# Kernel optimization log

Measured on AMD Instinct MI355X. Metric: run time of the kernel, lower is better.

## Reference

```python
import jax, jax.numpy as jnp
import numpy as np

EPS = 1e-5
D, H, W = 2, 4, 4          # fixed patch grid from the rearrange string
P = 8                       # p1*p2*p3 = 2*2*2 tokens per patch


def setup_inputs() -> dict:
    key = jax.random.key(0)
    k1, k2, k3, k4, k5 = jax.random.split(key, 5)
    c, heads = 128, 8
    B = 16 * D * H * W  # 512 patches (b=16)
    emb = jax.random.normal(k1, (B, P, c), dtype=jnp.float32)
    s = 1.0 / np.sqrt(c)
    Wq = jax.random.normal(k2, (c, c * heads), dtype=jnp.float32) * s
    Wk = jax.random.normal(k3, (c, c * heads), dtype=jnp.float32) * s
    Wv = jax.random.normal(k4, (c, c * heads), dtype=jnp.float32) * s
    Wout = jax.random.normal(k5, (c * heads, c), dtype=jnp.float32) * (1.0 / np.sqrt(c * heads))
    return {"emb": emb, "Wq": Wq, "Wk": Wk, "Wv": Wv, "Wout": Wout}


def reference(emb, Wq, Wk, Wv, Wout):
    B, n, c = emb.shape            # B = b*32, n = 8
    heads = Wq.shape[1] // c
    b = B // (D * H * W)

    q = emb @ Wq                   # (B, 8, c*heads)
    k = emb @ Wk
    v = emb @ Wv

    # '(p) (c heads)' -> heads c p  /  heads p c
    mh_q = q.reshape(B, P, c, heads).transpose(0, 3, 2, 1)   # (B, heads, c, P)
    mh_k = k.reshape(B, P, c, heads).transpose(0, 3, 1, 2)   # (B, heads, P, c)
    mh_v = v.reshape(B, P, c, heads).transpose(0, 3, 2, 1)   # (B, heads, c, P)

    attn = jnp.einsum('bhcp,bhpe->bhce', mh_q, mh_k)         # (B, heads, c, c) channel scores

    # InstanceNorm2d(num_heads): normalize each (patch, head) c x c map (biased var)
    mu = attn.mean(axis=(2, 3), keepdims=True)
    var = attn.var(axis=(2, 3), keepdims=True)
    attn = (attn - mu) * jax.lax.rsqrt(var + EPS)

    attn = jax.nn.softmax(attn, axis=3)
    ctx = jnp.einsum('bhce,bhep->bhcp', attn, mh_v)          # (B, heads, c, P)

    # '(b d h w) heads c (p1 p2 p3) -> b (d p1 h p2 w p3) (c heads)'
    ctx = ctx.reshape(b, D, H, W, heads, c, 2, 2, 2)
    ctx = ctx.transpose(0, 1, 6, 2, 7, 3, 8, 5, 4)           # b d p1 h p2 w p3 c heads
    ctx = ctx.reshape(b, D * 2 * H * 2 * W * 2, c * heads)   # (b, 256, c*heads)

    return ctx @ Wout                                        # (b, 256, c)
```

## Files before the change

kernel.cpp:

```cpp
#include <hip/hip_runtime.h>
#include <hip/hip_bf16.h>
#include <math.h>


typedef short bfrag __attribute__((ext_vector_type(8)));
typedef float f32x4 __attribute__((ext_vector_type(4)));

static __device__ __forceinline__ short f2bf(float x) {
    __hip_bfloat16 h = __float2bfloat16(x);
    return __builtin_bit_cast(short, h);
}
static __device__ __forceinline__ bfrag bzero() {
    bfrag z;
    #pragma unroll
    for (int j = 0; j < 8; ++j) z[j] = 0;
    return z;
}

__global__ __launch_bounds__(256) void convertW(
    const float* __restrict__ Wq, const float* __restrict__ Wk,
    const float* __restrict__ Wv, const float* __restrict__ Wout,
    short* __restrict__ Wp, short* __restrict__ Wout_pt,
    float* __restrict__ out)
{
    __shared__ short lt[128 * 33];
    const int b = blockIdx.x, t = threadIdx.x;

    {
        float4* o4 = (float4*)out;
        const int zb = b * 1024 + t;
        #pragma unroll
        for (int k = 0; k < 4; ++k)
            o4[zb + k * 256] = make_float4(0.f, 0.f, 0.f, 0.f);
    }

    if (b < 96) {
        const int x = b >> 5, h = (b >> 2) & 7, k0 = (b & 3) * 32;
        const float* W = (x == 0) ? Wq : (x == 1) ? Wk : Wv;
        #pragma unroll 4
        for (int rr = 0; rr < 16; ++rr) {
            const int k = rr * 2 + (t >> 7);
            const int i = t & 127;
            lt[k * 129 + i] = f2bf(W[(k0 + k) * 1024 + i * 8 + h]);
        }
        __syncthreads();
        short* dst = Wp + (x * 8 + h) * 16384;
        #pragma unroll
        for (int pp = 0; pp < 4; ++pp) {
            const int i  = pp * 32 + (t >> 3);
            const int kk = (t & 7) * 4;
            short4 v;
            v.x = lt[(kk + 0) * 129 + i]; v.y = lt[(kk + 1) * 129 + i];
            v.z = lt[(kk + 2) * 129 + i]; v.w = lt[(kk + 3) * 129 + i];
            *(short4*)&dst[i * 128 + k0 + kk] = v;
        }
    } else {
        const int b2 = b - 96, h = b2 >> 2, c0 = (b2 & 3) * 32;
        #pragma unroll 4
        for (int rr = 0; rr < 16; ++rr) {
            const int i = rr * 8 + (t >> 5);
            const int c = t & 31;
            lt[i * 33 + c] = f2bf(Wout[(i * 8 + h) * 128 + c0 + c]);
        }
        __syncthreads();
        short* dst = Wout_pt + h * 16384;
        #pragma unroll
        for (int pp = 0; pp < 4; ++pp) {
            const int c  = pp * 8 + (t >> 5);
            const int i0 = (t & 31) * 4;
            short4 v;
            v.x = lt[(i0 + 0) * 33 + c]; v.y = lt[(i0 + 1) * 33 + c];
            v.z = lt[(i0 + 2) * 33 + c]; v.w = lt[(i0 + 3) * 33 + c];
            *(short4*)&dst[(c0 + c) * 128 + i0] = v;
        }
    }
}

#define QT   0
#define KT   4096
#define QN   8192
#define KN   12288
#define VS   16384
#define CTXK 4096

__global__ __launch_bounds__(256, 4) void attn4(
    const float* __restrict__ emb,
    const short* __restrict__ Wp,
    const short* __restrict__ Wout_pt,
    float* __restrict__ out)
{
    __shared__ short lds[20480];
    const int bid = blockIdx.x;
    const int pg  = bid & 127;
    const int h   = bid >> 7;
    const int t   = threadIdx.x;
    const int w    = t >> 6;
    const int lane = t & 63;
    const int m16  = lane & 15;
    const int quad = lane >> 4;
    const int q8   = quad * 8;

    {
        bfrag a[2][4];
        #pragma unroll
        for (int tm = 0; tm < 2; ++tm)
            #pragma unroll
            for (int ks = 0; ks < 4; ++ks) {
                const float* er = emb + (size_t)(pg*32 + tm*16 + m16) * 128 + ks*32 + q8;
                const float4 x0 = *(const float4*)er;
                const float4 x1 = *(const float4*)(er + 4);
                bfrag f;
                f[0]=f2bf(x0.x); f[1]=f2bf(x0.y); f[2]=f2bf(x0.z); f[3]=f2bf(x0.w);
                f[4]=f2bf(x1.x); f[5]=f2bf(x1.y); f[6]=f2bf(x1.z); f[7]=f2bf(x1.w);
                a[tm][ks] = f;
            }

        #pragma unroll
        for (int tt = 0; tt < 6; ++tt) {
            const int nt = w * 6 + tt;
            const int x  = nt >> 3;
            const int i0 = (nt & 7) * 16;
            const short* Wb = Wp + ((x*8 + h)*128 + i0 + m16) * 128;
            bfrag bb[4];
            #pragma unroll
            for (int ks = 0; ks < 4; ++ks)
                bb[ks] = *(const bfrag*)&Wb[ks*32 + q8];
            f32x4 c0 = {0.f,0.f,0.f,0.f}, c1 = {0.f,0.f,0.f,0.f};
            __builtin_amdgcn_s_setprio(1);
            #pragma unroll
            for (int ks = 0; ks < 4; ++ks) {
                c0 = __builtin_amdgcn_mfma_f32_16x16x32_bf16(a[0][ks], bb[ks], c0, 0,0,0);
                c1 = __builtin_amdgcn_mfma_f32_16x16x32_bf16(a[1][ks], bb[ks], c1, 0,0,0);
            }
            __builtin_amdgcn_s_setprio(0);
            #pragma unroll
            for (int tm = 0; tm < 2; ++tm) {
                const f32x4 cc = tm ? c1 : c0;
                const int mrow0 = tm*16 + quad*4;
                const int pl = mrow0 >> 3;
                const int p0 = mrow0 & 7;
                const int col = i0 + m16;
                const int cb  = nt & 7;
                if (x == 0) {
                    short4 v;
                    v.x = f2bf(cc[0]); v.y = f2bf(cc[1]);
                    v.z = f2bf(cc[2]); v.w = f2bf(cc[3]);
                    *(short4*)&lds[QT + pl*1024 + col*8 + p0] = v;
                    #pragma unroll
                    for (int r = 0; r < 4; ++r)
                        lds[QN + pl*1024 + (p0 + r)*128
                            + ((cb ^ ((p0 + r) & 3)) << 4) + m16] = f2bf(cc[r]);
                } else if (x == 1) {
                    short4 v;
                    v.x = f2bf(cc[0]); v.y = f2bf(cc[1]);
                    v.z = f2bf(cc[2]); v.w = f2bf(cc[3]);
                    *(short4*)&lds[KT + pl*1024 + col*8 + p0] = v;
                    #pragma unroll
                    for (int r = 0; r < 4; ++r)
                        lds[KN + pl*1024 + (p0 + r)*128
                            + ((cb ^ ((p0 + r) & 3)) << 4) + m16] = f2bf(cc[r]);
                } else {
                    const int g = ((cb ^ (((pl & 1) << 1) | (p0 >> 2))) << 4);
                    #pragma unroll
                    for (int r = 0; r < 4; ++r)
                        lds[VS + pl*1024 + (p0 + r)*128 + g + m16] = f2bf(cc[r]);
                }
            }
        }
    }
    __syncthreads();

    float rs2, nbias;
    {
        bfrag gq[4], gk[4], gs[4], ones;
        #pragma unroll
        for (int j = 0; j < 8; ++j) ones[j] = (short)0x3F80;
        #pragma unroll
        for (int ks = 0; ks < 4; ++ks) {
            const int bswz = (((2*ks + (quad >> 1)) ^ (m16 & 3)) << 4) + (quad & 1)*8;
            gq[ks] = (m16 < 8) ? *(const bfrag*)&lds[QN + w*1024 + m16*128 + bswz] : bzero();
            gk[ks] = (m16 < 8) ? *(const bfrag*)&lds[KN + w*1024 + m16*128 + bswz] : bzero();
            gs[ks] = (m16 < 8) ? *(const bfrag*)&lds[QN + w*1024 + m16*128 + bswz]
                               : *(const bfrag*)&lds[KN + w*1024 + (m16 - 8)*128 + bswz];
        }
        f32x4 cg = {0.f,0.f,0.f,0.f}, ch = {0.f,0.f,0.f,0.f}, cs = {0.f,0.f,0.f,0.f};
        __builtin_amdgcn_s_setprio(1);
        #pragma unroll
        for (int ks = 0; ks < 4; ++ks) {
            cg = __builtin_amdgcn_mfma_f32_16x16x32_bf16(gq[ks], gq[ks], cg, 0,0,0);
            ch = __builtin_amdgcn_mfma_f32_16x16x32_bf16(gk[ks], gk[ks], ch, 0,0,0);
            cs = __builtin_amdgcn_mfma_f32_16x16x32_bf16(gs[ks], ones,  cs, 0,0,0);
        }
        __builtin_amdgcn_s_setprio(0);
        float gh = 0.f, sp = 0.f;
        #pragma unroll
        for (int r = 0; r < 4; ++r) {
            gh = fmaf(cg[r], ch[r], gh);
            sp = fmaf(cs[r], __shfl_xor(cs[r], 32), sp);
        }
        sp += __shfl_xor(sp, 16);
        #pragma unroll
        for (int off = 1; off <= 32; off <<= 1)
            gh += __shfl_xor(gh, off);
        const float mean = sp * (1.f / 16384.f);
        const float var  = gh * (1.f / 16384.f) - mean * mean;
        rs2   = rsqrtf(var + 1e-5f) * 1.44269504f;
        nbias = -mean * rs2;
    }

    bfrag bs[8], av[4];
    #pragma unroll
    for (int nt = 0; nt < 8; ++nt)
        bs[nt] = (quad == 0) ? *(const bfrag*)&lds[QT + w*1024 + (nt*16 + m16)*8] : bzero();
    #pragma unroll
    for (int ks = 0; ks < 4; ++ks) {
        if (m16 < 8) {
            const int g = (((2*ks + (quad >> 1)) ^ (((w & 1) << 1) | (m16 >> 2))) << 4);
            av[ks] = *(const bfrag*)&lds[VS + w*1024 + m16*128 + g + (quad & 1)*8];
        } else if (m16 == 8) {
            bfrag o;
            #pragma unroll
            for (int j = 0; j < 8; ++j) o[j] = (short)0x3F80;
            av[ks] = o;
        } else
            av[ks] = bzero();
    }

    const int key2 = m16 >> 2;
    const int rowoff = m16 * 32;
    const int pw = w * 1024 + rowoff;
    f32x4 cc[8];
    #pragma unroll
    for (int nt = 0; nt < 8; ++nt) cc[nt] = (f32x4){0.f,0.f,0.f,0.f};

    #pragma unroll
    for (int ks = 0; ks < 4; ++ks) {
        #pragma unroll
        for (int jb = 0; jb < 2; ++jb) {
            const int band = ks*2 + jb;
            const bfrag amk = (quad == 0)
                ? *(const bfrag*)&lds[KT + w*1024 + (band*16 + m16)*8] : bzero();
            const int tw = (((jb*2 + (quad >> 1)) ^ key2) << 3) + (quad & 1)*4;
            #pragma unroll
            for (int nt = 0; nt < 8; ++nt) {
                const int zb = (nt >> 1) == 0 ? QT : (nt >> 1) == 1 ? QN
                             : (nt >> 1) == 2 ? KN : VS;
                f32x4 z = {0.f,0.f,0.f,0.f};
                __builtin_amdgcn_s_setprio(1);
                const f32x4 s4 = __builtin_amdgcn_mfma_f32_16x16x32_bf16(amk, bs[nt], z, 0,0,0);
                __builtin_amdgcn_s_setprio(0);
                short4 v;
                v.x = f2bf(__builtin_amdgcn_exp2f(fmaf(s4[0], rs2, nbias)));
                v.y = f2bf(__builtin_amdgcn_exp2f(fmaf(s4[1], rs2, nbias)));
                v.z = f2bf(__builtin_amdgcn_exp2f(fmaf(s4[2], rs2, nbias)));
                v.w = f2bf(__builtin_amdgcn_exp2f(fmaf(s4[3], rs2, nbias)));
                *(short4*)&lds[zb + pw + (nt & 1)*512 + tw] = v;
            }
        }
        __builtin_amdgcn_s_setprio(1);
        #pragma unroll
        for (int nt = 0; nt < 8; ++nt) {
            const int zb = (nt >> 1) == 0 ? QT : (nt >> 1) == 1 ? QN
                         : (nt >> 1) == 2 ? KN : VS;
            const bfrag bp = *(const bfrag*)
                &lds[zb + pw + (nt & 1)*512 + ((quad ^ key2) << 3)];
            cc[nt] = __builtin_amdgcn_mfma_f32_16x16x32_bf16(av[ks], bp, cc[nt], 0,0,0);
        }
        __builtin_amdgcn_s_setprio(0);
    }

    #pragma unroll
    for (int nt = 0; nt < 8; ++nt) {
        const float s  = __shfl(cc[nt][0], 32 + m16);
        const float is = 1.0f / s;
        if (quad < 2) {
            #pragma unroll
            for (int r = 0; r < 4; ++r) {
                const int p = quad*4 + r;
                lds[CTXK + w*1024 + p*128 + ((nt ^ (p & 3)) << 4) + m16] =
                    f2bf(cc[nt][r] * is);
            }
        }
    }

    bfrag ac[4];
    #pragma unroll
    for (int ks = 0; ks < 4; ++ks)
        ac[ks] = (m16 < 8)
            ? *(const bfrag*)&lds[CTXK + w*1024 + m16*128
                  + (((2*ks + (quad >> 1)) ^ (m16 & 3)) << 4) + (quad & 1)*8]
            : bzero();
    const short* Wo = Wout_pt + h * 16384;
    const int pat = pg*4 + w;
    const int bb2 = pat >> 5, rem = pat & 31;
    const int dd = rem >> 4, hh2 = (rem >> 2) & 3, ww2 = rem & 3;

    bfrag wbA[4], wbB[4];
    #pragma unroll
    for (int ks = 0; ks < 4; ++ks)
        wbA[ks] = *(const bfrag*)&Wo[m16*128 + ks*32 + q8];
    #pragma unroll 1
    for (int nt = 0; nt < 8; ++nt) {
        if (nt < 7) {
            #pragma unroll
            for (int ks = 0; ks < 4; ++ks)
                wbB[ks] = *(const bfrag*)&Wo[((nt+1)*16 + m16)*128 + ks*32 + q8];
        }
        f32x4 cc2 = {0.f,0.f,0.f,0.f};
        __builtin_amdgcn_s_setprio(1);
        #pragma unroll
        for (int ks = 0; ks < 4; ++ks)
            cc2 = __builtin_amdgcn_mfma_f32_16x16x32_bf16(ac[ks], wbA[ks], cc2, 0,0,0);
        __builtin_amdgcn_s_setprio(0);
        if (quad < 2) {
            #pragma unroll
            for (int r = 0; r < 4; ++r) {
                const int orow = bb2*256
                    + ((((dd*2 + quad)*4 + hh2)*2 + (r >> 1))*4 + ww2)*2 + (r & 1);
                atomicAdd(&out[(size_t)orow*128 + nt*16 + m16], cc2[r]);
            }
        }
        #pragma unroll
        for (int ks = 0; ks < 4; ++ks)
            wbA[ks] = wbB[ks];
    }
}

extern "C" void kernel_launch(void* const* d_in, const int* in_sizes, int n_in,
                              void* d_out, int out_size, void* d_ws, size_t ws_size,
                              hipStream_t stream) {
    const float* emb  = (const float*)d_in[0];
    const float* Wq   = (const float*)d_in[1];
    const float* Wk   = (const float*)d_in[2];
    const float* Wv   = (const float*)d_in[3];
    const float* Wout = (const float*)d_in[4];
    float* out = (float*)d_out;

    short* Wp      = (short*)d_ws;
    short* Wout_pt = Wp + 393216;

    convertW<<<128, 256, 0, stream>>>(Wq, Wk, Wv, Wout, Wp, Wout_pt, out);
    attn4<<<1024, 256, 0, stream>>>(emb, Wp, Wout_pt, out);
}
```

Before: 101.4 us.

## Split each patch-head across two waves instead of four patches per block

After: 136.5 us. 34.6% more time.

```diff
diff --git a/kernel.cpp b/kernel.cpp
--- a/kernel.cpp
+++ b/kernel.cpp
@@ -76,23 +76,22 @@
     }
 }
 
-#define QT   0
-#define KT   4096
-#define QN   8192
-#define KN   12288
-#define VS   16384
-#define CTXK 4096
-
-__global__ __launch_bounds__(256, 4) void attn4(
+#define QT2  0
+#define KT2  1024
+#define QN2  2048
+#define KN2  3072
+#define VS2  4096
+
+__global__ __launch_bounds__(128, 6) void attn4(
     const float* __restrict__ emb,
     const short* __restrict__ Wp,
     const short* __restrict__ Wout_pt,
     float* __restrict__ out)
 {
-    __shared__ short lds[20480];
+    __shared__ short lds[5120];
     const int bid = blockIdx.x;
-    const int pg  = bid & 127;
-    const int h   = bid >> 7;
+    const int pt  = bid & 511;
+    const int h   = bid >> 9;
     const int t   = threadIdx.x;
     const int w    = t >> 6;
     const int lane = t & 63;
@@ -101,23 +100,24 @@
     const int q8   = quad * 8;
 
     {
-        bfrag a[2][4];
-        #pragma unroll
-        for (int tm = 0; tm < 2; ++tm)
-            #pragma unroll
-            for (int ks = 0; ks < 4; ++ks) {
-                const float* er = emb + (size_t)(pg*32 + tm*16 + m16) * 128 + ks*32 + q8;
+        bfrag a[4];
+        #pragma unroll
+        for (int ks = 0; ks < 4; ++ks) {
+            if (m16 < 8) {
+                const float* er = emb + (size_t)(pt*8 + m16) * 128 + ks*32 + q8;
                 const float4 x0 = *(const float4*)er;
                 const float4 x1 = *(const float4*)(er + 4);
                 bfrag f;
                 f[0]=f2bf(x0.x); f[1]=f2bf(x0.y); f[2]=f2bf(x0.z); f[3]=f2bf(x0.w);
                 f[4]=f2bf(x1.x); f[5]=f2bf(x1.y); f[6]=f2bf(x1.z); f[7]=f2bf(x1.w);
-                a[tm][ks] = f;
-            }
-
-        #pragma unroll
-        for (int tt = 0; tt < 6; ++tt) {
-            const int nt = w * 6 + tt;
+                a[ks] = f;
+            } else
+                a[ks] = bzero();
+        }
+
+        #pragma unroll 1
+        for (int tt = 0; tt < 12; ++tt) {
+            const int nt = w * 12 + tt;
             const int x  = nt >> 3;
             const int i0 = (nt & 7) * 16;
             const short* Wb = Wp + ((x*8 + h)*128 + i0 + m16) * 128;
@@ -125,45 +125,35 @@
             #pragma unroll
             for (int ks = 0; ks < 4; ++ks)
                 bb[ks] = *(const bfrag*)&Wb[ks*32 + q8];
-            f32x4 c0 = {0.f,0.f,0.f,0.f}, c1 = {0.f,0.f,0.f,0.f};
+            f32x4 c0 = {0.f,0.f,0.f,0.f};
             __builtin_amdgcn_s_setprio(1);
             #pragma unroll
-            for (int ks = 0; ks < 4; ++ks) {
-                c0 = __builtin_amdgcn_mfma_f32_16x16x32_bf16(a[0][ks], bb[ks], c0, 0,0,0);
-                c1 = __builtin_amdgcn_mfma_f32_16x16x32_bf16(a[1][ks], bb[ks], c1, 0,0,0);
-            }
+            for (int ks = 0; ks < 4; ++ks)
+                c0 = __builtin_amdgcn_mfma_f32_16x16x32_bf16(a[ks], bb[ks], c0, 0,0,0);
             __builtin_amdgcn_s_setprio(0);
-            #pragma unroll
-            for (int tm = 0; tm < 2; ++tm) {
-                const f32x4 cc = tm ? c1 : c0;
-                const int mrow0 = tm*16 + quad*4;
-                const int pl = mrow0 >> 3;
-                const int p0 = mrow0 & 7;
-                const int col = i0 + m16;
-                const int cb  = nt & 7;
+            if (quad < 2) {
+                const int p0 = quad * 4;
+                const int cb = nt & 7;
                 if (x == 0) {
                     short4 v;
-                    v.x = f2bf(cc[0]); v.y = f2bf(cc[1]);
-                    v.z = f2bf(cc[2]); v.w = f2bf(cc[3]);
-                    *(short4*)&lds[QT + pl*1024 + col*8 + p0] = v;
+                    v.x = f2bf(c0[0]); v.y = f2bf(c0[1]);
+                    v.z = f2bf(c0[2]); v.w = f2bf(c0[3]);
+                    *(short4*)&lds[QT2 + (i0 + m16)*8 + p0] = v;
                     #pragma unroll
                     for (int r = 0; r < 4; ++r)
-                        lds[QN + pl*1024 + (p0 + r)*128
-                            + ((cb ^ ((p0 + r) & 3)) << 4) + m16] = f2bf(cc[r]);
+                        lds[QN2 + (p0 + r)*128 + ((cb ^ r) << 4) + m16] = f2bf(c0[r]);
                 } else if (x == 1) {
                     short4 v;
-                    v.x = f2bf(cc[0]); v.y = f2bf(cc[1]);
-                    v.z = f2bf(cc[2]); v.w = f2bf(cc[3]);
-                    *(short4*)&lds[KT + pl*1024 + col*8 + p0] = v;
+                    v.x = f2bf(c0[0]); v.y = f2bf(c0[1]);
+                    v.z = f2bf(c0[2]); v.w = f2bf(c0[3]);
+                    *(short4*)&lds[KT2 + (i0 + m16)*8 + p0] = v;
                     #pragma unroll
                     for (int r = 0; r < 4; ++r)
-                        lds[KN + pl*1024 + (p0 + r)*128
-                            + ((cb ^ ((p0 + r) & 3)) << 4) + m16] = f2bf(cc[r]);
+                        lds[KN2 + (p0 + r)*128 + ((cb ^ r) << 4) + m16] = f2bf(c0[r]);
                 } else {
-                    const int g = ((cb ^ (((pl & 1) << 1) | (p0 >> 2))) << 4);
                     #pragma unroll
                     for (int r = 0; r < 4; ++r)
-                        lds[VS + pl*1024 + (p0 + r)*128 + g + m16] = f2bf(cc[r]);
+                        lds[VS2 + (p0 + r)*128 + ((cb ^ quad) << 4) + m16] = f2bf(c0[r]);
                 }
             }
         }
@@ -178,10 +168,10 @@
         #pragma unroll
         for (int ks = 0; ks < 4; ++ks) {
             const int bswz = (((2*ks + (quad >> 1)) ^ (m16 & 3)) << 4) + (quad & 1)*8;
-            gq[ks] = (m16 < 8) ? *(const bfrag*)&lds[QN + w*1024 + m16*128 + bswz] : bzero();
-            gk[ks] = (m16 < 8) ? *(const bfrag*)&lds[KN + w*1024 + m16*128 + bswz] : bzero();
-            gs[ks] = (m16 < 8) ? *(const bfrag*)&lds[QN + w*1024 + m16*128 + bswz]
-                               : *(const bfrag*)&lds[KN + w*1024 + (m16 - 8)*128 + bswz];
+            gq[ks] = (m16 < 8) ? *(const bfrag*)&lds[QN2 + m16*128 + bswz] : bzero();
+            gk[ks] = (m16 < 8) ? *(const bfrag*)&lds[KN2 + m16*128 + bswz] : bzero();
+            gs[ks] = (m16 < 8) ? *(const bfrag*)&lds[QN2 + m16*128 + bswz]
+                               : *(const bfrag*)&lds[KN2 + (m16 - 8)*128 + bswz];
         }
         f32x4 cg = {0.f,0.f,0.f,0.f}, ch = {0.f,0.f,0.f,0.f}, cs = {0.f,0.f,0.f,0.f};
         __builtin_amdgcn_s_setprio(1);
@@ -208,15 +198,16 @@
         nbias = -mean * rs2;
     }
 
-    bfrag bs[8], av[4];
-    #pragma unroll
-    for (int nt = 0; nt < 8; ++nt)
-        bs[nt] = (quad == 0) ? *(const bfrag*)&lds[QT + w*1024 + (nt*16 + m16)*8] : bzero();
+    bfrag bs[4], av[4];
+    #pragma unroll
+    for (int nt = 0; nt < 4; ++nt)
+        bs[nt] = (quad == 0)
+            ? *(const bfrag*)&lds[QT2 + (w*64 + nt*16 + m16)*8] : bzero();
     #pragma unroll
     for (int ks = 0; ks < 4; ++ks) {
         if (m16 < 8) {
-            const int g = (((2*ks + (quad >> 1)) ^ (((w & 1) << 1) | (m16 >> 2))) << 4);
-            av[ks] = *(const bfrag*)&lds[VS + w*1024 + m16*128 + g + (quad & 1)*8];
+            const int g = (((2*ks + (quad >> 1)) ^ (m16 >> 2)) << 4) + (quad & 1)*8;
+            av[ks] = *(const bfrag*)&lds[VS2 + m16*128 + g];
         } else if (m16 == 8) {
             bfrag o;
             #pragma unroll
@@ -225,13 +216,13 @@
         } else
             av[ks] = bzero();
     }
+    __syncthreads();
 
     const int key2 = m16 >> 2;
     const int rowoff = m16 * 32;
-    const int pw = w * 1024 + rowoff;
-    f32x4 cc[8];
-    #pragma unroll
-    for (int nt = 0; nt < 8; ++nt) cc[nt] = (f32x4){0.f,0.f,0.f,0.f};
+    f32x4 cc[4];
+    #pragma unroll
+    for (int nt = 0; nt < 4; ++nt) cc[nt] = (f32x4){0.f,0.f,0.f,0.f};
 
     #pragma unroll
     for (int ks = 0; ks < 4; ++ks) {
@@ -239,12 +230,12 @@
         for (int jb = 0; jb < 2; ++jb) {
             const int band = ks*2 + jb;
             const bfrag amk = (quad == 0)
-                ? *(const bfrag*)&lds[KT + w*1024 + (band*16 + m16)*8] : bzero();
+                ? *(const bfrag*)&lds[KT2 + (band*16 + m16)*8] : bzero();
             const int tw = (((jb*2 + (quad >> 1)) ^ key2) << 3) + (quad & 1)*4;
             #pragma unroll
-            for (int nt = 0; nt < 8; ++nt) {
-                const int zb = (nt >> 1) == 0 ? QT : (nt >> 1) == 1 ? QN
-                             : (nt >> 1) == 2 ? KN : VS;
+            for (int nt = 0; nt < 4; ++nt) {
+                const int pbase = (w == 0) ? ((nt >> 1) ? QN2 : QT2)
+                                           : ((nt >> 1) ? VS2 : KN2);
                 f32x4 z = {0.f,0.f,0.f,0.f};
                 __builtin_amdgcn_s_setprio(1);
                 const f32x4 s4 = __builtin_amdgcn_mfma_f32_16x16x32_bf16(amk, bs[nt], z, 0,0,0);
@@ -254,57 +245,60 @@
                 v.y = f2bf(__builtin_amdgcn_exp2f(fmaf(s4[1], rs2, nbias)));
                 v.z = f2bf(__builtin_amdgcn_exp2f(fmaf(s4[2], rs2, nbias)));
                 v.w = f2bf(__builtin_amdgcn_exp2f(fmaf(s4[3], rs2, nbias)));
-                *(short4*)&lds[zb + pw + (nt & 1)*512 + tw] = v;
+                *(short4*)&lds[pbase + (nt & 1)*512 + rowoff + tw] = v;
             }
         }
         __builtin_amdgcn_s_setprio(1);
         #pragma unroll
-        for (int nt = 0; nt < 8; ++nt) {
-            const int zb = (nt >> 1) == 0 ? QT : (nt >> 1) == 1 ? QN
-                         : (nt >> 1) == 2 ? KN : VS;
+        for (int nt = 0; nt < 4; ++nt) {
+            const int pbase = (w == 0) ? ((nt >> 1) ? QN2 : QT2)
+                                       : ((nt >> 1) ? VS2 : KN2);
             const bfrag bp = *(const bfrag*)
-                &lds[zb + pw + (nt & 1)*512 + ((quad ^ key2) << 3)];
+                &lds[pbase + (nt & 1)*512 + rowoff + ((quad ^ key2) << 3)];
             cc[nt] = __builtin_amdgcn_mfma_f32_16x16x32_bf16(av[ks], bp, cc[nt], 0,0,0);
         }
         __builtin_amdgcn_s_setprio(0);
     }
 
-    #pragma unroll
-    for (int nt = 0; nt < 8; ++nt) {
+    __syncthreads();
+
+    #pragma unroll
+    for (int nt = 0; nt < 4; ++nt) {
         const float s  = __shfl(cc[nt][0], 32 + m16);
         const float is = 1.0f / s;
         if (quad < 2) {
             #pragma unroll
             for (int r = 0; r < 4; ++r) {
                 const int p = quad*4 + r;
-                lds[CTXK + w*1024 + p*128 + ((nt ^ (p & 3)) << 4) + m16] =
+                lds[p*128 + (((w*4 + nt) ^ (p & 3)) << 4) + m16] =
                     f2bf(cc[nt][r] * is);
             }
         }
     }
+    __syncthreads();
 
     bfrag ac[4];
     #pragma unroll
     for (int ks = 0; ks < 4; ++ks)
         ac[ks] = (m16 < 8)
-            ? *(const bfrag*)&lds[CTXK + w*1024 + m16*128
+            ? *(const bfrag*)&lds[m16*128
                   + (((2*ks + (quad >> 1)) ^ (m16 & 3)) << 4) + (quad & 1)*8]
             : bzero();
     const short* Wo = Wout_pt + h * 16384;
-    const int pat = pg*4 + w;
-    const int bb2 = pat >> 5, rem = pat & 31;
+    const int bb2 = pt >> 5, rem = pt & 31;
     const int dd = rem >> 4, hh2 = (rem >> 2) & 3, ww2 = rem & 3;
 
     bfrag wbA[4], wbB[4];
     #pragma unroll
     for (int ks = 0; ks < 4; ++ks)
-        wbA[ks] = *(const bfrag*)&Wo[m16*128 + ks*32 + q8];
+        wbA[ks] = *(const bfrag*)&Wo[(w*64 + m16)*128 + ks*32 + q8];
     #pragma unroll 1
-    for (int nt = 0; nt < 8; ++nt) {
-        if (nt < 7) {
+    for (int n = 0; n < 4; ++n) {
+        const int ct = w*4 + n;
+        if (n < 3) {
             #pragma unroll
             for (int ks = 0; ks < 4; ++ks)
-                wbB[ks] = *(const bfrag*)&Wo[((nt+1)*16 + m16)*128 + ks*32 + q8];
+                wbB[ks] = *(const bfrag*)&Wo[((ct+1)*16 + m16)*128 + ks*32 + q8];
         }
         f32x4 cc2 = {0.f,0.f,0.f,0.f};
         __builtin_amdgcn_s_setprio(1);
@@ -317,7 +311,7 @@
             for (int r = 0; r < 4; ++r) {
                 const int orow = bb2*256
                     + ((((dd*2 + quad)*4 + hh2)*2 + (r >> 1))*4 + ww2)*2 + (r & 1);
-                atomicAdd(&out[(size_t)orow*128 + nt*16 + m16], cc2[r]);
+                atomicAdd(&out[(size_t)orow*128 + ct*16 + m16], cc2[r]);
             }
         }
         #pragma unroll
@@ -340,5 +334,5 @@
     short* Wout_pt = Wp + 393216;
 
     convertW<<<128, 256, 0, stream>>>(Wq, Wk, Wv, Wout, Wp, Wout_pt, out);
-    attn4<<<1024, 256, 0, stream>>>(emb, Wp, Wout_pt, out);
-}
+    attn4<<<4096, 128, 0, stream>>>(emb, Wp, Wout_pt, out);
+}
```

## Split each patch's attention across two waves with 512-thread blocks

Applied to the files above, without the earlier changes.

Result: slower. 145.2 us (+43.1%).

```diff
diff --git a/kernel.cpp b/kernel.cpp
--- a/kernel.cpp
+++ b/kernel.cpp
@@ -83,7 +83,7 @@
 #define VS   16384
 #define CTXK 4096
 
-__global__ __launch_bounds__(256, 4) void attn4(
+__global__ __launch_bounds__(512, 8) void attn4(
     const float* __restrict__ emb,
     const short* __restrict__ Wp,
     const short* __restrict__ Wout_pt,
@@ -94,7 +94,9 @@
     const int pg  = bid & 127;
     const int h   = bid >> 7;
     const int t   = threadIdx.x;
-    const int w    = t >> 6;
+    const int w8   = t >> 6;
+    const int plw  = w8 >> 1;
+    const int ih   = w8 & 1;
     const int lane = t & 63;
     const int m16  = lane & 15;
     const int quad = lane >> 4;
@@ -116,8 +118,8 @@
             }
 
         #pragma unroll
-        for (int tt = 0; tt < 6; ++tt) {
-            const int nt = w * 6 + tt;
+        for (int tt = 0; tt < 3; ++tt) {
+            const int nt = w8 * 3 + tt;
             const int x  = nt >> 3;
             const int i0 = (nt & 7) * 16;
             const short* Wb = Wp + ((x*8 + h)*128 + i0 + m16) * 128;
@@ -178,10 +180,10 @@
         #pragma unroll
         for (int ks = 0; ks < 4; ++ks) {
             const int bswz = (((2*ks + (quad >> 1)) ^ (m16 & 3)) << 4) + (quad & 1)*8;
-            gq[ks] = (m16 < 8) ? *(const bfrag*)&lds[QN + w*1024 + m16*128 + bswz] : bzero();
-            gk[ks] = (m16 < 8) ? *(const bfrag*)&lds[KN + w*1024 + m16*128 + bswz] : bzero();
-            gs[ks] = (m16 < 8) ? *(const bfrag*)&lds[QN + w*1024 + m16*128 + bswz]
-                               : *(const bfrag*)&lds[KN + w*1024 + (m16 - 8)*128 + bswz];
+            gq[ks] = (m16 < 8) ? *(const bfrag*)&lds[QN + plw*1024 + m16*128 + bswz] : bzero();
+            gk[ks] = (m16 < 8) ? *(const bfrag*)&lds[KN + plw*1024 + m16*128 + bswz] : bzero();
+            gs[ks] = (m16 < 8) ? *(const bfrag*)&lds[QN + plw*1024 + m16*128 + bswz]
+                               : *(const bfrag*)&lds[KN + plw*1024 + (m16 - 8)*128 + bswz];
         }
         f32x4 cg = {0.f,0.f,0.f,0.f}, ch = {0.f,0.f,0.f,0.f}, cs = {0.f,0.f,0.f,0.f};
         __builtin_amdgcn_s_setprio(1);
@@ -208,15 +210,16 @@
         nbias = -mean * rs2;
     }
 
-    bfrag bs[8], av[4];
-    #pragma unroll
-    for (int nt = 0; nt < 8; ++nt)
-        bs[nt] = (quad == 0) ? *(const bfrag*)&lds[QT + w*1024 + (nt*16 + m16)*8] : bzero();
+    bfrag bs[4], av[4];
+    #pragma unroll
+    for (int nt = 0; nt < 4; ++nt)
+        bs[nt] = (quad == 0)
+            ? *(const bfrag*)&lds[QT + plw*1024 + (ih*64 + nt*16 + m16)*8] : bzero();
     #pragma unroll
     for (int ks = 0; ks < 4; ++ks) {
         if (m16 < 8) {
-            const int g = (((2*ks + (quad >> 1)) ^ (((w & 1) << 1) | (m16 >> 2))) << 4);
-            av[ks] = *(const bfrag*)&lds[VS + w*1024 + m16*128 + g + (quad & 1)*8];
+            const int g = (((2*ks + (quad >> 1)) ^ (((plw & 1) << 1) | (m16 >> 2))) << 4);
+            av[ks] = *(const bfrag*)&lds[VS + plw*1024 + m16*128 + g + (quad & 1)*8];
         } else if (m16 == 8) {
             bfrag o;
             #pragma unroll
@@ -225,13 +228,13 @@
         } else
             av[ks] = bzero();
     }
+    __syncthreads();
 
     const int key2 = m16 >> 2;
     const int rowoff = m16 * 32;
-    const int pw = w * 1024 + rowoff;
-    f32x4 cc[8];
-    #pragma unroll
-    for (int nt = 0; nt < 8; ++nt) cc[nt] = (f32x4){0.f,0.f,0.f,0.f};
+    f32x4 cc[4];
+    #pragma unroll
+    for (int nt = 0; nt < 4; ++nt) cc[nt] = (f32x4){0.f,0.f,0.f,0.f};
 
     #pragma unroll
     for (int ks = 0; ks < 4; ++ks) {
@@ -239,12 +242,12 @@
         for (int jb = 0; jb < 2; ++jb) {
             const int band = ks*2 + jb;
             const bfrag amk = (quad == 0)
-                ? *(const bfrag*)&lds[KT + w*1024 + (band*16 + m16)*8] : bzero();
+                ? *(const bfrag*)&lds[KT + plw*1024 + (band*16 + m16)*8] : bzero();
             const int tw = (((jb*2 + (quad >> 1)) ^ key2) << 3) + (quad & 1)*4;
             #pragma unroll
-            for (int nt = 0; nt < 8; ++nt) {
-                const int zb = (nt >> 1) == 0 ? QT : (nt >> 1) == 1 ? QN
-                             : (nt >> 1) == 2 ? KN : VS;
+            for (int nt = 0; nt < 4; ++nt) {
+                const int zb = (ih == 0) ? ((nt >> 1) ? QN : QT)
+                                         : ((nt >> 1) ? VS : KN);
                 f32x4 z = {0.f,0.f,0.f,0.f};
                 __builtin_amdgcn_s_setprio(1);
                 const f32x4 s4 = __builtin_amdgcn_mfma_f32_16x16x32_bf16(amk, bs[nt], z, 0,0,0);
@@ -254,57 +257,61 @@
                 v.y = f2bf(__builtin_amdgcn_exp2f(fmaf(s4[1], rs2, nbias)));
                 v.z = f2bf(__builtin_amdgcn_exp2f(fmaf(s4[2], rs2, nbias)));
                 v.w = f2bf(__builtin_amdgcn_exp2f(fmaf(s4[3], rs2, nbias)));
-                *(short4*)&lds[zb + pw + (nt & 1)*512 + tw] = v;
+                *(short4*)&lds[zb + plw*1024 + (nt & 1)*512 + rowoff + tw] = v;
             }
         }
         __builtin_amdgcn_s_setprio(1);
         #pragma unroll
-        for (int nt = 0; nt < 8; ++nt) {
-            const int zb = (nt >> 1) == 0 ? QT : (nt >> 1) == 1 ? QN
-                         : (nt >> 1) == 2 ? KN : VS;
+        for (int nt = 0; nt < 4; ++nt) {
+            const int zb = (ih == 0) ? ((nt >> 1) ? QN : QT)
+                                     : ((nt >> 1) ? VS : KN);
             const bfrag bp = *(const bfrag*)
-                &lds[zb + pw + (nt & 1)*512 + ((quad ^ key2) << 3)];
+                &lds[zb + plw*1024 + (nt & 1)*512 + rowoff + ((quad ^ key2) << 3)];
             cc[nt] = __builtin_amdgcn_mfma_f32_16x16x32_bf16(av[ks], bp, cc[nt], 0,0,0);
         }
         __builtin_amdgcn_s_setprio(0);
     }
 
-    #pragma unroll
-    for (int nt = 0; nt < 8; ++nt) {
+    __syncthreads();
+
+    #pragma unroll
+    for (int nt = 0; nt < 4; ++nt) {
         const float s  = __shfl(cc[nt][0], 32 + m16);
         const float is = 1.0f / s;
         if (quad < 2) {
             #pragma unroll
             for (int r = 0; r < 4; ++r) {
                 const int p = quad*4 + r;
-                lds[CTXK + w*1024 + p*128 + ((nt ^ (p & 3)) << 4) + m16] =
+                lds[CTXK + plw*1024 + p*128 + (((ih*4 + nt) ^ (p & 3)) << 4) + m16] =
                     f2bf(cc[nt][r] * is);
             }
         }
     }
+    __syncthreads();
 
     bfrag ac[4];
     #pragma unroll
     for (int ks = 0; ks < 4; ++ks)
         ac[ks] = (m16 < 8)
-            ? *(const bfrag*)&lds[CTXK + w*1024 + m16*128
+            ? *(const bfrag*)&lds[CTXK + plw*1024 + m16*128
                   + (((2*ks + (quad >> 1)) ^ (m16 & 3)) << 4) + (quad & 1)*8]
             : bzero();
     const short* Wo = Wout_pt + h * 16384;
-    const int pat = pg*4 + w;
+    const int pat = pg*4 + plw;
     const int bb2 = pat >> 5, rem = pat & 31;
     const int dd = rem >> 4, hh2 = (rem >> 2) & 3, ww2 = rem & 3;
 
     bfrag wbA[4], wbB[4];
     #pragma unroll
     for (int ks = 0; ks < 4; ++ks)
-        wbA[ks] = *(const bfrag*)&Wo[m16*128 + ks*32 + q8];
+        wbA[ks] = *(const bfrag*)&Wo[(ih*64 + m16)*128 + ks*32 + q8];
     #pragma unroll 1
-    for (int nt = 0; nt < 8; ++nt) {
-        if (nt < 7) {
+    for (int n = 0; n < 4; ++n) {
+        const int ct = ih*4 + n;
+        if (n < 3) {
             #pragma unroll
             for (int ks = 0; ks < 4; ++ks)
-                wbB[ks] = *(const bfrag*)&Wo[((nt+1)*16 + m16)*128 + ks*32 + q8];
+                wbB[ks] = *(const bfrag*)&Wo[((ct+1)*16 + m16)*128 + ks*32 + q8];
         }
         f32x4 cc2 = {0.f,0.f,0.f,0.f};
         __builtin_amdgcn_s_setprio(1);
@@ -317,7 +324,7 @@
             for (int r = 0; r < 4; ++r) {
                 const int orow = bb2*256
                     + ((((dd*2 + quad)*4 + hh2)*2 + (r >> 1))*4 + ww2)*2 + (r & 1);
-                atomicAdd(&out[(size_t)orow*128 + nt*16 + m16], cc2[r]);
+                atomicAdd(&out[(size_t)orow*128 + ct*16 + m16], cc2[r]);
             }
         }
         #pragma unroll
@@ -340,5 +347,5 @@
     short* Wout_pt = Wp + 393216;
 
     convertW<<<128, 256, 0, stream>>>(Wq, Wk, Wv, Wout, Wp, Wout_pt, out);
-    attn4<<<1024, 256, 0, stream>>>(emb, Wp, Wout_pt, out);
-}
+    attn4<<<1024, 512, 0, stream>>>(emb, Wp, Wout_pt, out);
+}
```
